# Kernel optimization log

Hardware: AMD Instinct MI355X
Metric: run time of the kernel (lower is better)

## Reference

```python
import jax, jax.numpy as jnp
import numpy as np

N_HEADS = 16

def setup_inputs() -> dict:
    key = jax.random.key(0)
    kx, kk, kq, kv, ko = jax.random.split(key, 5)
    B, T, D = 8, 1024, 1024
    s = 1.0 / np.sqrt(D)
    return {
        'x':  jax.random.normal(kx, (B, T, D), dtype=jnp.float32),
        'Wk': jax.random.normal(kk, (D, D), dtype=jnp.float32) * s,
        'Wq': jax.random.normal(kq, (D, D), dtype=jnp.float32) * s,
        'Wv': jax.random.normal(kv, (D, D), dtype=jnp.float32) * s,
        'Wo': jax.random.normal(ko, (D, D), dtype=jnp.float32) * s,
    }

def reference(x, Wk, Wq, Wv, Wo):
    B, T, D = x.shape
    H = D // N_HEADS  # head dim
    # projections (nn.Linear with bias=False: y = x @ W^T)
    k = (x @ Wk.T).reshape(B, T, N_HEADS, H).transpose(0, 2, 1, 3)  # [B,n,T,H]
    q = (x @ Wq.T).reshape(B, T, N_HEADS, H).transpose(0, 2, 1, 3)
    v = (x @ Wv.T).reshape(B, T, N_HEADS, H).transpose(0, 2, 1, 3)
    scores = jnp.einsum('bnqh,bnkh->bnqk', q, k)                    # [B,n,T,T]
    causal = jnp.tril(jnp.ones((T, T), dtype=bool))
    # original: masked_fill(-inf) BEFORE scaling; -inf/sqrt(H) stays -inf
    scores = jnp.where(causal, scores, -jnp.inf) / jnp.sqrt(jnp.float32(H))
    att = jax.nn.softmax(scores, axis=-1)
    # dropout p=0.0 -> identity
    out = jnp.einsum('bnqk,bnkh->bnqh', att, v)                     # [B,n,T,H]
    out = out.transpose(0, 2, 1, 3).reshape(B, T, D)
    return out @ Wo.T
```

## Files before the change

### kernel.cpp

```cpp
#include <hip/hip_runtime.h>
#include <stdint.h>

typedef __bf16 bf16x8 __attribute__((ext_vector_type(8)));
typedef float f32x4 __attribute__((ext_vector_type(4)));
typedef unsigned short ushort_t;
typedef unsigned int uint_t;

__device__ inline ushort_t f2bf(float f) {
  uint_t u = __builtin_bit_cast(uint_t, f);
  u = (u + 0x7FFFu + ((u >> 16) & 1u)) >> 16;
  return (ushort_t)u;
}

__device__ inline void gll16(const void* g, void* l) {
  __builtin_amdgcn_global_load_lds(
      (__attribute__((address_space(1))) void*)(uintptr_t)g,
      (__attribute__((address_space(3))) void*)(uint32_t)(uintptr_t)l,
      16, 0, 0);
}

__global__ void cast_all(const float* __restrict__ x, const float* __restrict__ w0,
                         const float* __restrict__ w1, const float* __restrict__ w2,
                         const float* __restrict__ w3, ushort_t* __restrict__ xb,
                         ushort_t* __restrict__ wc, float s0) {
  const int i = blockIdx.x * 256 + threadIdx.x;
  const float* src;
  ushort_t* dst;
  float sc = 1.0f;
  int j;
  if (i < (1 << 21)) {
    src = x;
    dst = xb;
    j = i;
  } else {
    const int k = i - (1 << 21);
    const int which = k >> 18;
    src = which == 0 ? w0 : which == 1 ? w1 : which == 2 ? w2 : w3;
    if (which == 0) sc = s0;
    dst = wc + (k >> 18) * (1 << 20);
    j = k & 0x3FFFF;
  }
  float4 v = reinterpret_cast<const float4*>(src)[j];
  ushort4 o;
  o.x = f2bf(v.x * sc);
  o.y = f2bf(v.y * sc);
  o.z = f2bf(v.z * sc);
  o.w = f2bf(v.w * sc);
  reinterpret_cast<ushort4*>(dst)[j] = o;
}

#define MFMA16(A_, B_, C_) __builtin_amdgcn_mfma_f32_16x16x32_bf16(A_, B_, C_, 0, 0, 0)
#define SBAR __builtin_amdgcn_s_barrier
#define SCHED0 __builtin_amdgcn_sched_barrier(0)

template <int MF, int NF, int NTN, int LDC, bool F32OUT>
__global__ __launch_bounds__(512, 2) void gemm8p(const ushort_t* __restrict__ A,
                                                 const ushort_t* __restrict__ B,
                                                 void* __restrict__ C) {
  constexpr int BM = MF * 32;
  constexpr int BN = NF * 64;
  constexpr int NA = BM / 64;
  constexpr int NB = BN / 64;
  constexpr int AU = BM * 64;
  constexpr int BUF = AU + BN * 64;
  constexpr int NWG = (8192 / BM) * NTN;
  __shared__ __attribute__((aligned(16))) ushort_t smem[2 * BUF];

  const int tid = threadIdx.x;
  const int lane = tid & 63;
  const int w = tid >> 6;
  const int wm = w >> 2, wn = w & 3;

  const int bid = blockIdx.x;
  const int swz = (bid & 7) * (NWG / 8) + (bid >> 3);
  const int m0 = (swz / NTN) * BM;
  const int n0 = (swz % NTN) * BN;

  const int scol = ((tid & 7) ^ ((tid >> 3) & 7)) * 8;
  const ushort_t* gA = A + (size_t)(m0 + (tid >> 3)) * 1024 + scol;
  const ushort_t* gB = B + (size_t)(n0 + (tid >> 3)) * 1024 + scol;

  const int lr = lane & 15;
  const int hi = lane >> 4;
  const int arow = (wm * MF * 16 + lr) * 64;
  const int brow = AU + (wn * NF * 16 + lr) * 64;
  const int cx0 = (hi * 8) ^ ((lane & 7) << 3);
  const int cx1 = cx0 ^ 32;

  f32x4 acc[MF][NF] = {};
  bf16x8 a0[MF / 2][2], a1[MF / 2][2];
  bf16x8 b[NF][2];

  auto stage_all = [&](int wbu, int sk) __attribute__((always_inline)) {
#pragma unroll
    for (int i = 0; i < NA; ++i)
      gll16(gA + i * 65536 + sk, &smem[wbu + i * 4096 + (w << 9)]);
#pragma unroll
    for (int i = 0; i < NB; ++i)
      gll16(gB + i * 65536 + sk, &smem[wbu + AU + i * 4096 + (w << 9)]);
  };
  auto rdA = [&](int rbu, int mbase, bf16x8(&aa)[MF / 2][2])
      __attribute__((always_inline)) {
#pragma unroll
    for (int m = 0; m < MF / 2; ++m) {
      const int base = rbu + arow + (mbase + m) * 1024;
      aa[m][0] = *(const bf16x8*)&smem[base + cx0];
      aa[m][1] = *(const bf16x8*)&smem[base + cx1];
    }
  };
  auto rdBall = [&](int rbu) __attribute__((always_inline)) {
#pragma unroll
    for (int n = 0; n < NF; ++n) {
      const int base = rbu + brow + n * 1024;
      b[n][0] = *(const bf16x8*)&smem[base + cx0];
      b[n][1] = *(const bf16x8*)&smem[base + cx1];
    }
  };
  auto mmH = [&](int mbase, bf16x8(&aa)[MF / 2][2]) __attribute__((always_inline)) {
#pragma unroll
    for (int m = 0; m < MF / 2; ++m)
#pragma unroll
      for (int n = 0; n < NF; ++n) {
        acc[mbase + m][n] = MFMA16(aa[m][0], b[n][0], acc[mbase + m][n]);
        acc[mbase + m][n] = MFMA16(aa[m][1], b[n][1], acc[mbase + m][n]);
      }
  };

  auto tile = [&](int rbu, int wbu, int sk, bool pf) __attribute__((always_inline)) {
    rdA(rbu, 0, a0);
    rdBall(rbu);
    if (pf) stage_all(wbu, sk);
    rdA(rbu, MF / 2, a1);
    SCHED0;
    __builtin_amdgcn_s_setprio(1);
    mmH(0, a0);
    __builtin_amdgcn_s_setprio(0);
    SCHED0;
    __builtin_amdgcn_s_setprio(1);
    mmH(MF / 2, a1);
    __builtin_amdgcn_s_setprio(0);
    SCHED0;
    if (pf) asm volatile("s_waitcnt vmcnt(0)" ::: "memory");
    SBAR();
    SCHED0;
  };

  stage_all(0, 0);
  asm volatile("s_waitcnt vmcnt(0)" ::: "memory");
  SBAR();
  SCHED0;
  int sk = 64;
  for (int it = 0; it < 7; ++it) {
    tile(0, BUF, sk, true);
    sk += 64;
    tile(BUF, 0, sk, true);
    sk += 64;
  }
  tile(0, BUF, sk, true);
  tile(BUF, 0, 0, false);

  const size_t erow = (size_t)(m0 + wm * MF * 16 + hi * 4);
  const int ecol = n0 + wn * NF * 16 + lr;
#pragma unroll
  for (int mf = 0; mf < MF; ++mf)
#pragma unroll
    for (int nf = 0; nf < NF; ++nf)
#pragma unroll
      for (int r = 0; r < 4; ++r) {
        const size_t idx = (erow + mf * 16 + r) * LDC + ecol + nf * 16;
        if constexpr (F32OUT)
          ((float*)C)[idx] = acc[mf][nf][r];
        else
          ((ushort_t*)C)[idx] = f2bf(acc[mf][nf][r]);
      }
}

__global__ __launch_bounds__(256, 2) void attn_fwd(const ushort_t* __restrict__ QKV,
                                                   ushort_t* __restrict__ ctx) {
  const int bid = blockIdx.x;
  const int h = bid & 15;
  const int b = (bid >> 4) & 7;
  const int p = bid >> 7;
  const int tid = threadIdx.x;
  const int lane = tid & 63;
  const int w = tid >> 6;
  const int lr = lane & 15;
  const int lg = lane >> 4;
  const int dk = lg << 3;

  __shared__ __attribute__((aligned(16))) ushort_t Ks[2][64 * 72];
  __shared__ __attribute__((aligned(16))) uint_t VtDw[2][64 * 36];

  const int kkey = tid >> 2, kdg = tid & 3;
  const int vkp = tid & 31, vdg = tid >> 5;
  const int pkp = ((vkp >> 4) << 4) | (((vkp >> 1) & 3) << 2) |
                  (((vkp >> 3) & 1) << 1) | (vkp & 1);
  const ushort_t* kgbase =
      QKV + ((size_t)(b * 1024 + kkey)) * 3072 + 1024 + h * 64 + kdg * 16;
  const ushort_t* vgbase =
      QKV + ((size_t)(b * 1024 + 2 * vkp)) * 3072 + 2048 + h * 64 + vdg * 8;

  const float FMAX2 = 23.083120654223414f;

  const int qtA = p, qtB = 7 - p;
  const int ntB = (qtB + 1) << 1;
  const int wrow0A = (qtA << 7) + w * 32;
  const int wrow0B = (qtB << 7) + w * 32;

  bf16x8 qfA[2][2], qfB[2][2];
#pragma unroll
  for (int i = 0; i < 2; ++i) {
    const ushort_t* qpA =
        QKV + ((size_t)(b * 1024 + wrow0A + i * 16 + lr)) * 3072 + h * 64 + dk;
    qfA[i][0] = *reinterpret_cast<const bf16x8*>(qpA);
    qfA[i][1] = *reinterpret_cast<const bf16x8*>(qpA + 32);
    const ushort_t* qpB =
        QKV + ((size_t)(b * 1024 + wrow0B + i * 16 + lr)) * 3072 + h * 64 + dk;
    qfB[i][0] = *reinterpret_cast<const bf16x8*>(qpB);
    qfB[i][1] = *reinterpret_cast<const bf16x8*>(qpB + 32);
  }

  f32x4 oA[2][4] = {}, oB[2][4] = {};
  float lsA[2] = {0.f, 0.f}, lsB[2] = {0.f, 0.f};

  uint4 rk0 = *reinterpret_cast<const uint4*>(kgbase);
  uint4 rk1 = *reinterpret_cast<const uint4*>(kgbase + 8);
  uint4 rv0 = *reinterpret_cast<const uint4*>(vgbase);
  uint4 rv1 = *reinterpret_cast<const uint4*>(vgbase + 3072);

  for (int t = 0; t < ntB; ++t) {
    const int bsel = t & 1;
    asm volatile("s_waitcnt vmcnt(0)" ::: "memory");
    {
      uint_t* kd = reinterpret_cast<uint_t*>(&Ks[bsel][kkey * 72 + kdg * 16]);
      *reinterpret_cast<uint4*>(kd) = rk0;
      *reinterpret_cast<uint4*>(kd + 4) = rk1;
      const ushort_t* e0 = reinterpret_cast<const ushort_t*>(&rv0);
      const ushort_t* e1 = reinterpret_cast<const ushort_t*>(&rv1);
#pragma unroll
      for (int j = 0; j < 8; ++j)
        VtDw[bsel][(vdg * 8 + j) * 36 + pkp] = (uint_t)e0[j] | ((uint_t)e1[j] << 16);
    }
    if (t + 1 < ntB) {
      const size_t off = (size_t)(t + 1) * 64 * 3072;
      rk0 = *reinterpret_cast<const uint4*>(kgbase + off);
      rk1 = *reinterpret_cast<const uint4*>(kgbase + off + 8);
      rv0 = *reinterpret_cast<const uint4*>(vgbase + off);
      rv1 = *reinterpret_cast<const uint4*>(vgbase + off + 3072);
    }
    asm volatile("s_waitcnt lgkmcnt(0)" ::: "memory");
    __builtin_amdgcn_s_barrier();

    const int kb = t << 6;
    const bool actB = (kb <= wrow0B + 31);
    const bool actA = (kb <= wrow0A + 31);
    if (!(actA || actB)) continue;

    bf16x8 kf0[4], kf1[4];
#pragma unroll
    for (int f = 0; f < 4; ++f) {
      kf0[f] = *reinterpret_cast<const bf16x8*>(&Ks[bsel][(f * 16 + lr) * 72 + dk]);
      kf1[f] =
          *reinterpret_cast<const bf16x8*>(&Ks[bsel][(f * 16 + lr) * 72 + 32 + dk]);
    }
    bf16x8 vb[2][4];
#pragma unroll
    for (int kblk = 0; kblk < 2; ++kblk)
#pragma unroll
      for (int fh = 0; fh < 4; ++fh)
        vb[kblk][fh] = *reinterpret_cast<const bf16x8*>(
            &VtDw[bsel][(fh * 16 + lr) * 36 + kblk * 16 + (lg << 2)]);

    auto group = [&](const bf16x8(&qf)[2][2], f32x4(&o)[2][4], float(&ls)[2],
                     int wrow0) __attribute__((always_inline)) {
      f32x4 s[2][4];
      __builtin_amdgcn_s_setprio(1);
#pragma unroll
      for (int i = 0; i < 2; ++i)
#pragma unroll
        for (int f = 0; f < 4; ++f) {
          f32x4 z = {0.f, 0.f, 0.f, 0.f};
          z = __builtin_amdgcn_mfma_f32_16x16x32_bf16(kf0[f], qf[i][0], z, 0, 0, 0);
          s[i][f] = __builtin_amdgcn_mfma_f32_16x16x32_bf16(kf1[f], qf[i][1], z, 0, 0, 0);
        }
      __builtin_amdgcn_s_setprio(0);
      const bool needmask = (kb + 63 > wrow0);
#pragma unroll
      for (int i = 0; i < 2; ++i) {
        const int qr = wrow0 + i * 16 + lr;
        uint_t d0[4], d1[4];
#pragma unroll
        for (int f = 0; f < 4; ++f) {
          const int kbase = kb + f * 16 + (lg << 2);
          float p0 = __builtin_amdgcn_exp2f(s[i][f][0] - FMAX2);
          float p1 = __builtin_amdgcn_exp2f(s[i][f][1] - FMAX2);
          float p2 = __builtin_amdgcn_exp2f(s[i][f][2] - FMAX2);
          float p3 = __builtin_amdgcn_exp2f(s[i][f][3] - FMAX2);
          if (needmask) {
            p0 = (kbase + 0 <= qr) ? p0 : 0.f;
            p1 = (kbase + 1 <= qr) ? p1 : 0.f;
            p2 = (kbase + 2 <= qr) ? p2 : 0.f;
            p3 = (kbase + 3 <= qr) ? p3 : 0.f;
          }
          ls[i] += (p0 + p1) + (p2 + p3);
          asm("v_cvt_pk_bf16_f32 %0, %1, %2" : "=v"(d0[f]) : "v"(p0), "v"(p1));
          asm("v_cvt_pk_bf16_f32 %0, %1, %2" : "=v"(d1[f]) : "v"(p2), "v"(p3));
        }
        __builtin_amdgcn_s_setprio(1);
#pragma unroll
        for (int kblk = 0; kblk < 2; ++kblk) {
          uint4 paw;
          paw.x = d0[2 * kblk];
          paw.y = d1[2 * kblk];
          paw.z = d0[2 * kblk + 1];
          paw.w = d1[2 * kblk + 1];
          const bf16x8 pa = __builtin_bit_cast(bf16x8, paw);
#pragma unroll
          for (int fh = 0; fh < 4; ++fh)
            o[i][fh] = __builtin_amdgcn_mfma_f32_16x16x32_bf16(pa, vb[kblk][fh],
                                                               o[i][fh], 0, 0, 0);
        }
        __builtin_amdgcn_s_setprio(0);
      }
    };

    if (actB) group(qfB, oB, lsB, wrow0B);
    if (actA) group(qfA, oA, lsA, wrow0A);
  }

  auto epi = [&](f32x4(&o)[2][4], float(&ls)[2], int wrow0)
      __attribute__((always_inline)) {
#pragma unroll
    for (int i = 0; i < 2; ++i) {
      float s = ls[i];
      s += __shfl_xor(s, 16);
      s += __shfl_xor(s, 32);
      const float linv = 1.0f / s;
      const size_t crow = (size_t)(b * 1024 + wrow0 + i * 16 + (lg << 2));
#pragma unroll
      for (int r = 0; r < 4; ++r) {
        const float li = __shfl(linv, (lg << 2) + r);
#pragma unroll
        for (int fh = 0; fh < 4; ++fh)
          ctx[(crow + r) * 1024 + h * 64 + fh * 16 + lr] = f2bf(o[i][fh][r] * li);
      }
    }
  };
  epi(oB, lsB, wrow0B);
  epi(oA, lsA, wrow0A);
}

extern "C" void kernel_launch(void* const* d_in, const int* in_sizes, int n_in,
                              void* d_out, int out_size, void* d_ws, size_t ws_size,
                              hipStream_t stream) {
  const float* x = (const float*)d_in[0];
  const float* Wk = (const float*)d_in[1];
  const float* Wq = (const float*)d_in[2];
  const float* Wv = (const float*)d_in[3];
  const float* Wo = (const float*)d_in[4];

  char* ws = (char*)d_ws;
  ushort_t* xb = (ushort_t*)ws;
  ushort_t* Wc = (ushort_t*)(ws + (16u << 20));
  ushort_t* Wob = Wc + 3u * 1024 * 1024;
  ushort_t* QKV = (ushort_t*)(ws + (24u << 20));
  ushort_t* ctx = xb;

  cast_all<<<12288, 256, 0, stream>>>(x, Wq, Wk, Wv, Wo, xb, Wc,
                                      0.125f * 1.4426950408889634f);

  gemm8p<8, 3, 16, 3072, false><<<512, 512, 0, stream>>>(xb, Wc, QKV);

  attn_fwd<<<512, 256, 0, stream>>>(QKV, ctx);

  gemm8p<4, 2, 8, 1024, true><<<512, 512, 0, stream>>>(ctx, Wob, (float*)d_out);
}
```

Baseline: 123.3 us.

## Split paired query tiles across 8 waves in 512-thread attention blocks

The attention kernel now launches 512 threads per block. Waves 0-3 handle the high query tile and waves 4-7 the low tile, instead of each wave processing both tiles sequentially. K/V staging loads are halved per thread, and K fragments are loaded per f inside the score loop to cut register pressure. Launch bounds become (512,4) to raise occupancy. The tradeoffs are that waves on the short tile idle at barriers while the long tile continues, and more waves contend for the same LDS.

```diff
diff --git a/kernel.cpp b/kernel.cpp
--- a/kernel.cpp
+++ b/kernel.cpp
@@ -175,7 +175,7 @@
       }
 }
 
-__global__ __launch_bounds__(256, 2) void attn_fwd(const ushort_t* __restrict__ QKV,
+__global__ __launch_bounds__(512, 4) void attn_fwd(const ushort_t* __restrict__ QKV,
                                                    ushort_t* __restrict__ ctx) {
   const int bid = blockIdx.x;
   const int h = bid & 15;
@@ -191,99 +191,83 @@
   __shared__ __attribute__((aligned(16))) ushort_t Ks[2][64 * 72];
   __shared__ __attribute__((aligned(16))) uint_t VtDw[2][64 * 36];
 
-  const int kkey = tid >> 2, kdg = tid & 3;
+  const int krow = tid >> 3, kd8 = (tid & 7) << 3;
   const int vkp = tid & 31, vdg = tid >> 5;
   const int pkp = ((vkp >> 4) << 4) | (((vkp >> 1) & 3) << 2) |
                   (((vkp >> 3) & 1) << 1) | (vkp & 1);
   const ushort_t* kgbase =
-      QKV + ((size_t)(b * 1024 + kkey)) * 3072 + 1024 + h * 64 + kdg * 16;
+      QKV + ((size_t)(b * 1024 + krow)) * 3072 + 1024 + h * 64 + kd8;
   const ushort_t* vgbase =
-      QKV + ((size_t)(b * 1024 + 2 * vkp)) * 3072 + 2048 + h * 64 + vdg * 8;
+      QKV + ((size_t)(b * 1024 + 2 * vkp)) * 3072 + 2048 + h * 64 + vdg * 4;
 
   const float FMAX2 = 23.083120654223414f;
 
   const int qtA = p, qtB = 7 - p;
   const int ntB = (qtB + 1) << 1;
-  const int wrow0A = (qtA << 7) + w * 32;
-  const int wrow0B = (qtB << 7) + w * 32;
-
-  bf16x8 qfA[2][2], qfB[2][2];
+  const int qt = (w >> 2) ? qtA : qtB;
+  const int wrow0 = (qt << 7) + (w & 3) * 32;
+
+  bf16x8 qf[2][2];
 #pragma unroll
   for (int i = 0; i < 2; ++i) {
-    const ushort_t* qpA =
-        QKV + ((size_t)(b * 1024 + wrow0A + i * 16 + lr)) * 3072 + h * 64 + dk;
-    qfA[i][0] = *reinterpret_cast<const bf16x8*>(qpA);
-    qfA[i][1] = *reinterpret_cast<const bf16x8*>(qpA + 32);
-    const ushort_t* qpB =
-        QKV + ((size_t)(b * 1024 + wrow0B + i * 16 + lr)) * 3072 + h * 64 + dk;
-    qfB[i][0] = *reinterpret_cast<const bf16x8*>(qpB);
-    qfB[i][1] = *reinterpret_cast<const bf16x8*>(qpB + 32);
-  }
-
-  f32x4 oA[2][4] = {}, oB[2][4] = {};
-  float lsA[2] = {0.f, 0.f}, lsB[2] = {0.f, 0.f};
-
-  uint4 rk0 = *reinterpret_cast<const uint4*>(kgbase);
-  uint4 rk1 = *reinterpret_cast<const uint4*>(kgbase + 8);
-  uint4 rv0 = *reinterpret_cast<const uint4*>(vgbase);
-  uint4 rv1 = *reinterpret_cast<const uint4*>(vgbase + 3072);
+    const ushort_t* qp =
+        QKV + ((size_t)(b * 1024 + wrow0 + i * 16 + lr)) * 3072 + h * 64 + dk;
+    qf[i][0] = *reinterpret_cast<const bf16x8*>(qp);
+    qf[i][1] = *reinterpret_cast<const bf16x8*>(qp + 32);
+  }
+
+  f32x4 o[2][4] = {};
+  float ls[2] = {0.f, 0.f};
+
+  uint4 rk = *reinterpret_cast<const uint4*>(kgbase);
+  uint2 rva = *reinterpret_cast<const uint2*>(vgbase);
+  uint2 rvb = *reinterpret_cast<const uint2*>(vgbase + 3072);
 
   for (int t = 0; t < ntB; ++t) {
     const int bsel = t & 1;
     asm volatile("s_waitcnt vmcnt(0)" ::: "memory");
+    *reinterpret_cast<uint4*>(&Ks[bsel][krow * 72 + kd8]) = rk;
     {
-      uint_t* kd = reinterpret_cast<uint_t*>(&Ks[bsel][kkey * 72 + kdg * 16]);
-      *reinterpret_cast<uint4*>(kd) = rk0;
-      *reinterpret_cast<uint4*>(kd + 4) = rk1;
-      const ushort_t* e0 = reinterpret_cast<const ushort_t*>(&rv0);
-      const ushort_t* e1 = reinterpret_cast<const ushort_t*>(&rv1);
-#pragma unroll
-      for (int j = 0; j < 8; ++j)
-        VtDw[bsel][(vdg * 8 + j) * 36 + pkp] = (uint_t)e0[j] | ((uint_t)e1[j] << 16);
+      const ushort_t* ea = reinterpret_cast<const ushort_t*>(&rva);
+      const ushort_t* eb = reinterpret_cast<const ushort_t*>(&rvb);
+#pragma unroll
+      for (int j = 0; j < 4; ++j)
+        VtDw[bsel][(vdg * 4 + j) * 36 + pkp] = (uint_t)ea[j] | ((uint_t)eb[j] << 16);
     }
     if (t + 1 < ntB) {
       const size_t off = (size_t)(t + 1) * 64 * 3072;
-      rk0 = *reinterpret_cast<const uint4*>(kgbase + off);
-      rk1 = *reinterpret_cast<const uint4*>(kgbase + off + 8);
-      rv0 = *reinterpret_cast<const uint4*>(vgbase + off);
-      rv1 = *reinterpret_cast<const uint4*>(vgbase + off + 3072);
+      rk = *reinterpret_cast<const uint4*>(kgbase + off);
+      rva = *reinterpret_cast<const uint2*>(vgbase + off);
+      rvb = *reinterpret_cast<const uint2*>(vgbase + off + 3072);
     }
     asm volatile("s_waitcnt lgkmcnt(0)" ::: "memory");
     __builtin_amdgcn_s_barrier();
 
     const int kb = t << 6;
-    const bool actB = (kb <= wrow0B + 31);
-    const bool actA = (kb <= wrow0A + 31);
-    if (!(actA || actB)) continue;
-
-    bf16x8 kf0[4], kf1[4];
-#pragma unroll
-    for (int f = 0; f < 4; ++f) {
-      kf0[f] = *reinterpret_cast<const bf16x8*>(&Ks[bsel][(f * 16 + lr) * 72 + dk]);
-      kf1[f] =
-          *reinterpret_cast<const bf16x8*>(&Ks[bsel][(f * 16 + lr) * 72 + 32 + dk]);
-    }
-    bf16x8 vb[2][4];
-#pragma unroll
-    for (int kblk = 0; kblk < 2; ++kblk)
-#pragma unroll
-      for (int fh = 0; fh < 4; ++fh)
-        vb[kblk][fh] = *reinterpret_cast<const bf16x8*>(
-            &VtDw[bsel][(fh * 16 + lr) * 36 + kblk * 16 + (lg << 2)]);
-
-    auto group = [&](const bf16x8(&qf)[2][2], f32x4(&o)[2][4], float(&ls)[2],
-                     int wrow0) __attribute__((always_inline)) {
+    if (kb <= wrow0 + 31) {
       f32x4 s[2][4];
       __builtin_amdgcn_s_setprio(1);
 #pragma unroll
-      for (int i = 0; i < 2; ++i)
-#pragma unroll
-        for (int f = 0; f < 4; ++f) {
+      for (int f = 0; f < 4; ++f) {
+        const bf16x8 kf0 =
+            *reinterpret_cast<const bf16x8*>(&Ks[bsel][(f * 16 + lr) * 72 + dk]);
+        const bf16x8 kf1 =
+            *reinterpret_cast<const bf16x8*>(&Ks[bsel][(f * 16 + lr) * 72 + 32 + dk]);
+#pragma unroll
+        for (int i = 0; i < 2; ++i) {
           f32x4 z = {0.f, 0.f, 0.f, 0.f};
-          z = __builtin_amdgcn_mfma_f32_16x16x32_bf16(kf0[f], qf[i][0], z, 0, 0, 0);
-          s[i][f] = __builtin_amdgcn_mfma_f32_16x16x32_bf16(kf1[f], qf[i][1], z, 0, 0, 0);
+          z = __builtin_amdgcn_mfma_f32_16x16x32_bf16(kf0, qf[i][0], z, 0, 0, 0);
+          s[i][f] = __builtin_amdgcn_mfma_f32_16x16x32_bf16(kf1, qf[i][1], z, 0, 0, 0);
         }
+      }
       __builtin_amdgcn_s_setprio(0);
+      bf16x8 vb[2][4];
+#pragma unroll
+      for (int kblk = 0; kblk < 2; ++kblk)
+#pragma unroll
+        for (int fh = 0; fh < 4; ++fh)
+          vb[kblk][fh] = *reinterpret_cast<const bf16x8*>(
+              &VtDw[bsel][(fh * 16 + lr) * 36 + kblk * 16 + (lg << 2)]);
       const bool needmask = (kb + 63 > wrow0);
 #pragma unroll
       for (int i = 0; i < 2; ++i) {
@@ -322,32 +306,24 @@
         }
         __builtin_amdgcn_s_setprio(0);
       }
-    };
-
-    if (actB) group(qfB, oB, lsB, wrow0B);
-    if (actA) group(qfA, oA, lsA, wrow0A);
-  }
-
-  auto epi = [&](f32x4(&o)[2][4], float(&ls)[2], int wrow0)
-      __attribute__((always_inline)) {
-#pragma unroll
-    for (int i = 0; i < 2; ++i) {
-      float s = ls[i];
-      s += __shfl_xor(s, 16);
-      s += __shfl_xor(s, 32);
-      const float linv = 1.0f / s;
-      const size_t crow = (size_t)(b * 1024 + wrow0 + i * 16 + (lg << 2));
-#pragma unroll
-      for (int r = 0; r < 4; ++r) {
-        const float li = __shfl(linv, (lg << 2) + r);
-#pragma unroll
-        for (int fh = 0; fh < 4; ++fh)
-          ctx[(crow + r) * 1024 + h * 64 + fh * 16 + lr] = f2bf(o[i][fh][r] * li);
-      }
-    }
-  };
-  epi(oB, lsB, wrow0B);
-  epi(oA, lsA, wrow0A);
+    }
+  }
+
+#pragma unroll
+  for (int i = 0; i < 2; ++i) {
+    float s = ls[i];
+    s += __shfl_xor(s, 16);
+    s += __shfl_xor(s, 32);
+    const float linv = 1.0f / s;
+    const size_t crow = (size_t)(b * 1024 + wrow0 + i * 16 + (lg << 2));
+#pragma unroll
+    for (int r = 0; r < 4; ++r) {
+      const float li = __shfl(linv, (lg << 2) + r);
+#pragma unroll
+      for (int fh = 0; fh < 4; ++fh)
+        ctx[(crow + r) * 1024 + h * 64 + fh * 16 + lr] = f2bf(o[i][fh][r] * li);
+    }
+  }
 }
 
 extern "C" void kernel_launch(void* const* d_in, const int* in_sizes, int n_in,
@@ -371,7 +347,7 @@
 
   gemm8p<8, 3, 16, 3072, false><<<512, 512, 0, stream>>>(xb, Wc, QKV);
 
-  attn_fwd<<<512, 256, 0, stream>>>(QKV, ctx);
+  attn_fwd<<<512, 512, 0, stream>>>(QKV, ctx);
 
   gemm8p<4, 2, 8, 1024, true><<<512, 512, 0, stream>>>(ctx, Wob, (float*)d_out);
 }
```

Result: slower. 181.3 us (+47.1%).

## Split GEMM staging into quarter-tile loads interleaved with MFMA groups

Applied to the files above, without the earlier changes.

The GEMM main loop now stages each tile in four pieces (A first half, B first column-block, remaining B, A second half) with a permuted row mapping, so each MFMA group can start once only its own piece has landed. Partial vmcnt waits and extra barriers replace the single full wait at the end of the tile. The attention kernel also splits each 16-byte V register load into two 8-byte loads. The aim is to overlap global-to-LDS traffic with compute at a finer grain, at the cost of more barriers and more complex counter bookkeeping that could stall or be wrong.

```diff
diff --git a/kernel.cpp b/kernel.cpp
--- a/kernel.cpp
+++ b/kernel.cpp
@@ -52,6 +52,8 @@
 #define MFMA16(A_, B_, C_) __builtin_amdgcn_mfma_f32_16x16x32_bf16(A_, B_, C_, 0, 0, 0)
 #define SBAR __builtin_amdgcn_s_barrier
 #define SCHED0 __builtin_amdgcn_sched_barrier(0)
+#define LGKM0 asm volatile("s_waitcnt lgkmcnt(0)" ::: "memory")
+#define VMC(n) asm volatile("s_waitcnt vmcnt(" #n ")" ::: "memory")
 
 template <int MF, int NF, int NTN, int LDC, bool F32OUT>
 __global__ __launch_bounds__(512, 2) void gemm8p(const ushort_t* __restrict__ A,
@@ -60,7 +62,9 @@
   constexpr int BM = MF * 32;
   constexpr int BN = NF * 64;
   constexpr int NA = BM / 64;
-  constexpr int NB = BN / 64;
+  constexpr int NAH = NA / 2;
+  constexpr int NBR = NF - 1;
+  constexpr int QA = BM / 4;
   constexpr int AU = BM * 64;
   constexpr int BUF = AU + BN * 64;
   constexpr int NWG = (8192 / BM) * NTN;
@@ -76,14 +80,29 @@
   const int m0 = (swz / NTN) * BM;
   const int n0 = (swz % NTN) * BN;
 
-  const int scol = ((tid & 7) ^ ((tid >> 3) & 7)) * 8;
-  const ushort_t* gA = A + (size_t)(m0 + (tid >> 3)) * 1024 + scol;
-  const ushort_t* gB = B + (size_t)(n0 + (tid >> 3)) * 1024 + scol;
+  const int prow = tid >> 3;
+  const int scol = ((tid & 7) ^ (prow & 7)) * 8;
+  const ushort_t* gA0 = A + (size_t)m0 * 1024 + scol;
+  const ushort_t* gB0 = B + (size_t)n0 * 1024 + scol;
+
+  int arow_ld[NA];
+#pragma unroll
+  for (int i = 0; i < NA; ++i) {
+    const int half = (i >= NAH) ? 1 : 0;
+    const int p = (i - half * NAH) * 64 + prow;
+    arow_ld[i] = (p / QA) * (BM / 2) + half * QA + (p % QA);
+  }
+  const int brow0 = (prow >> 4) * (BN / 4) + (prow & 15);
+  int browr_ld[(NBR > 0) ? NBR : 1];
+#pragma unroll
+  for (int j = 0; j < NBR; ++j) {
+    const int p = j * 64 + prow;
+    constexpr int R = (NF - 1) * 16;
+    browr_ld[j] = (p / R) * (NF * 16) + 16 + (p % R);
+  }
 
   const int lr = lane & 15;
   const int hi = lane >> 4;
-  const int arow = (wm * MF * 16 + lr) * 64;
-  const int brow = AU + (wn * NF * 16 + lr) * 64;
   const int cx0 = (hi * 8) ^ ((lane & 7) << 3);
   const int cx1 = cx0 ^ 32;
 
@@ -91,64 +110,121 @@
   bf16x8 a0[MF / 2][2], a1[MF / 2][2];
   bf16x8 b[NF][2];
 
-  auto stage_all = [&](int wbu, int sk) __attribute__((always_inline)) {
-#pragma unroll
-    for (int i = 0; i < NA; ++i)
-      gll16(gA + i * 65536 + sk, &smem[wbu + i * 4096 + (w << 9)]);
-#pragma unroll
-    for (int i = 0; i < NB; ++i)
-      gll16(gB + i * 65536 + sk, &smem[wbu + AU + i * 4096 + (w << 9)]);
-  };
-  auto rdA = [&](int rbu, int mbase, bf16x8(&aa)[MF / 2][2])
+  auto stage_uA1 = [&](int wbu, int sk) __attribute__((always_inline)) {
+#pragma unroll
+    for (int i = 0; i < NAH; ++i)
+      gll16(gA0 + (size_t)arow_ld[i] * 1024 + sk, &smem[wbu + i * 4096 + (w << 9)]);
+  };
+  auto stage_uA2 = [&](int wbu, int sk) __attribute__((always_inline)) {
+#pragma unroll
+    for (int i = NAH; i < NA; ++i)
+      gll16(gA0 + (size_t)arow_ld[i] * 1024 + sk, &smem[wbu + i * 4096 + (w << 9)]);
+  };
+  auto stage_uB0 = [&](int wbu, int sk) __attribute__((always_inline)) {
+    gll16(gB0 + (size_t)brow0 * 1024 + sk, &smem[wbu + AU + (w << 9)]);
+  };
+  auto stage_uBr = [&](int wbu, int sk) __attribute__((always_inline)) {
+#pragma unroll
+    for (int j = 0; j < NBR; ++j)
+      gll16(gB0 + (size_t)browr_ld[j] * 1024 + sk,
+            &smem[wbu + AU + 4096 + j * 4096 + (w << 9)]);
+  };
+  auto rdAh = [&](int rbu, int half, bf16x8(&aa)[MF / 2][2])
       __attribute__((always_inline)) {
 #pragma unroll
     for (int m = 0; m < MF / 2; ++m) {
-      const int base = rbu + arow + (mbase + m) * 1024;
+      const int par = half * (BM / 2) + wm * QA + m * 16 + lr;
+      const int base = rbu + par * 64;
       aa[m][0] = *(const bf16x8*)&smem[base + cx0];
       aa[m][1] = *(const bf16x8*)&smem[base + cx1];
     }
   };
-  auto rdBall = [&](int rbu) __attribute__((always_inline)) {
-#pragma unroll
-    for (int n = 0; n < NF; ++n) {
-      const int base = rbu + brow + n * 1024;
+  auto rdB0 = [&](int rbu) __attribute__((always_inline)) {
+    const int pbr = wn * 16 + lr;
+    const int base = rbu + AU + pbr * 64;
+    b[0][0] = *(const bf16x8*)&smem[base + cx0];
+    b[0][1] = *(const bf16x8*)&smem[base + cx1];
+  };
+  auto rdBr = [&](int rbu) __attribute__((always_inline)) {
+#pragma unroll
+    for (int n = 1; n < NF; ++n) {
+      const int pbr = 64 + wn * (NF - 1) * 16 + (n - 1) * 16 + lr;
+      const int base = rbu + AU + pbr * 64;
       b[n][0] = *(const bf16x8*)&smem[base + cx0];
       b[n][1] = *(const bf16x8*)&smem[base + cx1];
     }
   };
-  auto mmH = [&](int mbase, bf16x8(&aa)[MF / 2][2]) __attribute__((always_inline)) {
+  auto mmg = [&](int mbase, int ng0, int ng1, bf16x8(&aa)[MF / 2][2])
+      __attribute__((always_inline)) {
 #pragma unroll
     for (int m = 0; m < MF / 2; ++m)
 #pragma unroll
       for (int n = 0; n < NF; ++n) {
+        if (n < ng0 || n >= ng1) continue;
         acc[mbase + m][n] = MFMA16(aa[m][0], b[n][0], acc[mbase + m][n]);
         acc[mbase + m][n] = MFMA16(aa[m][1], b[n][1], acc[mbase + m][n]);
       }
   };
 
   auto tile = [&](int rbu, int wbu, int sk, bool pf) __attribute__((always_inline)) {
-    rdA(rbu, 0, a0);
-    rdBall(rbu);
-    if (pf) stage_all(wbu, sk);
-    rdA(rbu, MF / 2, a1);
+    rdAh(rbu, 0, a0);
+    rdB0(rbu);
+    SCHED0;
+    if (pf) {
+      stage_uA1(wbu, sk);
+      if constexpr (NA == 4) VMC(4); else VMC(2);
+    } else {
+      if constexpr (NA == 4) VMC(2); else VMC(1);
+    }
+    SBAR();
+    LGKM0;
     SCHED0;
     __builtin_amdgcn_s_setprio(1);
-    mmH(0, a0);
+    mmg(0, 0, 1, a0);
     __builtin_amdgcn_s_setprio(0);
+    SBAR();
+    rdBr(rbu);
+    SCHED0;
+    if (pf) {
+      stage_uB0(wbu, sk);
+      if constexpr (NA == 4) VMC(3); else VMC(2);
+    } else {
+      VMC(0);
+    }
+    SBAR();
+    LGKM0;
     SCHED0;
     __builtin_amdgcn_s_setprio(1);
-    mmH(MF / 2, a1);
+    mmg(0, 1, NF, a0);
     __builtin_amdgcn_s_setprio(0);
-    SCHED0;
-    if (pf) asm volatile("s_waitcnt vmcnt(0)" ::: "memory");
-    SBAR();
-    SCHED0;
-  };
-
-  stage_all(0, 0);
-  asm volatile("s_waitcnt vmcnt(0)" ::: "memory");
+    SBAR();
+    rdAh(rbu, 1, a1);
+    SCHED0;
+    if (pf) stage_uBr(wbu, sk);
+    SBAR();
+    LGKM0;
+    SCHED0;
+    __builtin_amdgcn_s_setprio(1);
+    mmg(MF / 2, 1, NF, a1);
+    __builtin_amdgcn_s_setprio(0);
+    SBAR();
+    if (pf) {
+      stage_uA2(wbu, sk);
+      if constexpr (NA == 4) VMC(4); else VMC(2);
+    }
+    SBAR();
+    __builtin_amdgcn_s_setprio(1);
+    mmg(MF / 2, 0, 1, a1);
+    __builtin_amdgcn_s_setprio(0);
+    SBAR();
+  };
+
+  stage_uA1(0, 0);
+  stage_uB0(0, 0);
+  stage_uBr(0, 0);
+  stage_uA2(0, 0);
+  if constexpr (NA == 4) VMC(4); else VMC(2);
   SBAR();
-  SCHED0;
   int sk = 64;
   for (int it = 0; it < 7; ++it) {
     tile(0, BUF, sk, true);
@@ -225,8 +301,10 @@
 
   uint4 rk0 = *reinterpret_cast<const uint4*>(kgbase);
   uint4 rk1 = *reinterpret_cast<const uint4*>(kgbase + 8);
-  uint4 rv0 = *reinterpret_cast<const uint4*>(vgbase);
-  uint4 rv1 = *reinterpret_cast<const uint4*>(vgbase + 3072);
+  uint2 rva = *reinterpret_cast<const uint2*>(vgbase);
+  uint2 rvb = *reinterpret_cast<const uint2*>(vgbase + 4);
+  uint2 rvc = *reinterpret_cast<const uint2*>(vgbase + 3072);
+  uint2 rvd = *reinterpret_cast<const uint2*>(vgbase + 3072 + 4);
 
   for (int t = 0; t < ntB; ++t) {
     const int bsel = t & 1;
@@ -235,18 +313,25 @@
       uint_t* kd = reinterpret_cast<uint_t*>(&Ks[bsel][kkey * 72 + kdg * 16]);
       *reinterpret_cast<uint4*>(kd) = rk0;
       *reinterpret_cast<uint4*>(kd + 4) = rk1;
-      const ushort_t* e0 = reinterpret_cast<const ushort_t*>(&rv0);
-      const ushort_t* e1 = reinterpret_cast<const ushort_t*>(&rv1);
-#pragma unroll
-      for (int j = 0; j < 8; ++j)
-        VtDw[bsel][(vdg * 8 + j) * 36 + pkp] = (uint_t)e0[j] | ((uint_t)e1[j] << 16);
+      const ushort_t* e0a = reinterpret_cast<const ushort_t*>(&rva);
+      const ushort_t* e0b = reinterpret_cast<const ushort_t*>(&rvb);
+      const ushort_t* e1a = reinterpret_cast<const ushort_t*>(&rvc);
+      const ushort_t* e1b = reinterpret_cast<const ushort_t*>(&rvd);
+#pragma unroll
+      for (int j = 0; j < 4; ++j) {
+        VtDw[bsel][(vdg * 8 + j) * 36 + pkp] = (uint_t)e0a[j] | ((uint_t)e1a[j] << 16);
+        VtDw[bsel][(vdg * 8 + 4 + j) * 36 + pkp] =
+            (uint_t)e0b[j] | ((uint_t)e1b[j] << 16);
+      }
     }
     if (t + 1 < ntB) {
       const size_t off = (size_t)(t + 1) * 64 * 3072;
       rk0 = *reinterpret_cast<const uint4*>(kgbase + off);
       rk1 = *reinterpret_cast<const uint4*>(kgbase + off + 8);
-      rv0 = *reinterpret_cast<const uint4*>(vgbase + off);
-      rv1 = *reinterpret_cast<const uint4*>(vgbase + off + 3072);
+      rva = *reinterpret_cast<const uint2*>(vgbase + off);
+      rvb = *reinterpret_cast<const uint2*>(vgbase + off + 4);
+      rvc = *reinterpret_cast<const uint2*>(vgbase + off + 3072);
+      rvd = *reinterpret_cast<const uint2*>(vgbase + off + 3072 + 4);
     }
     asm volatile("s_waitcnt lgkmcnt(0)" ::: "memory");
     __builtin_amdgcn_s_barrier();
```

New measurement: 129.3 us. 4.9% more time.
